# Kernel tuning notes

Measured on AMD Instinct MI355X. Metric: run time of the kernel, lower is better.

The kernel has to match this reference:

```python
import jax, jax.numpy as jnp
import numpy as np

B, C, H, W = 8, 512, 64, 64
DEPTH, HEADS = 4, 8


def setup_inputs() -> dict:
    key = jax.random.key(0)
    ks = jax.random.split(key, 7)
    s = 0.02
    return {
        "x": jax.random.normal(ks[0], (B, C, H, W), jnp.float32),
        # axial positional embeddings, emb dim at index 1: (1,C,H,1) and (1,C,1,W)
        "pos_h": jax.random.normal(ks[1], (C, H), jnp.float32) * s,
        "pos_w": jax.random.normal(ks[2], (C, W), jnp.float32) * s,
        # per layer, per axis (0=height, 1=width): q, kv, out projections
        "wq": jax.random.normal(ks[3], (DEPTH, 2, C, C), jnp.float32) * s,
        "wkv": jax.random.normal(ks[4], (DEPTH, 2, C, 2 * C), jnp.float32) * s,
        "wo": jax.random.normal(ks[5], (DEPTH, 2, C, C), jnp.float32) * s,
        "wo_b": jax.random.normal(ks[6], (DEPTH, 2, C), jnp.float32) * s,
    }


def _attn_last_axis(x, wq, wkv, wo, wo_b, heads):
    """Self-attention along the second-to-last axis. x: (..., L, C)."""
    lead = x.shape[:-2]
    L, Cd = x.shape[-2], x.shape[-1]
    e = Cd // heads
    q = x @ wq                       # (..., L, C)
    k, v = jnp.split(x @ wkv, 2, axis=-1)
    sh = lead + (L, heads, e)
    q, k, v = q.reshape(sh), k.reshape(sh), v.reshape(sh)
    dots = jnp.einsum('...ihe,...jhe->...hij', q, k) * (e ** -0.5)
    attn = jax.nn.softmax(dots, axis=-1)
    out = jnp.einsum('...hij,...jhe->...ihe', attn, v).reshape(lead + (L, heads * e))
    return out @ wo + wo_b


def reference(x, pos_h, pos_w, wq, wkv, wo, wo_b):
    # positional embedding: x + (1,C,H,1) + (1,C,1,W)
    x = x + pos_h[None, :, :, None] + pos_w[None, :, None, :]
    y = jnp.transpose(x, (0, 2, 3, 1))  # (B,H,W,C) channels-last working layout
    for l in range(DEPTH):
        # height-axis attention: (B,W,H,C), attend along H
        yh = jnp.transpose(y, (0, 2, 1, 3))
        oh = _attn_last_axis(yh, wq[l, 0], wkv[l, 0], wo[l, 0], wo_b[l, 0], HEADS)
        oh = jnp.transpose(oh, (0, 2, 1, 3))
        # width-axis attention: attend along W
        ow = _attn_last_axis(y, wq[l, 1], wkv[l, 1], wo[l, 1], wo_b[l, 1], HEADS)
        y = oh + ow  # sum_axial_out=True, no residual
    return jnp.transpose(y, (0, 3, 1, 2))  # back to (B,C,H,W)
```

## Files before the change

kernel.cpp:

```cpp
#include <hip/hip_runtime.h>
#include <stdint.h>


typedef __attribute__((ext_vector_type(8))) short bf16x8;
typedef __attribute__((ext_vector_type(4))) float f32x4;
typedef unsigned short u16;
typedef unsigned int u32;

#define MFMA16(a, b, c) __builtin_amdgcn_mfma_f32_16x16x32_bf16((a), (b), (c), 0, 0, 0)

__device__ __forceinline__ float b2f(u16 h) {
    u32 u = ((u32)h) << 16;
    float f;
    __builtin_memcpy(&f, &u, 4);
    return f;
}
__device__ __forceinline__ u16 f2b(float f) {
    u32 u;
    __builtin_memcpy(&u, &f, 4);
    u32 r = (u + 0x7fffu + ((u >> 16) & 1u)) >> 16;
    return (u16)r;
}

#define GLD_LDS16(g, l)                                                        \
    __builtin_amdgcn_global_load_lds(                                          \
        (const __attribute__((address_space(1))) void*)(g),                    \
        (__attribute__((address_space(3))) void*)(l), 16, 0, 0)

__global__ __launch_bounds__(256) void embed_kernel(
    const float* __restrict__ x, const float* __restrict__ ph,
    const float* __restrict__ pw, u16* __restrict__ y)
{
    __shared__ float tile[64][65];
    const int c0 = blockIdx.x * 64, h = blockIdx.y, b = blockIdx.z;
    const int t = threadIdx.x;
#pragma unroll
    for (int i = 0; i < 4; ++i) {
        int cl = (t >> 4) + i * 16;
        int w4 = (t & 15) * 4;
        const float* src = x + (((size_t)(b * 512 + c0 + cl)) * 64 + h) * 64 + w4;
        float4 v = *(const float4*)src;
        float p = ph[(c0 + cl) * 64 + h];
        tile[cl][w4 + 0] = v.x + p + pw[(c0 + cl) * 64 + w4 + 0];
        tile[cl][w4 + 1] = v.y + p + pw[(c0 + cl) * 64 + w4 + 1];
        tile[cl][w4 + 2] = v.z + p + pw[(c0 + cl) * 64 + w4 + 2];
        tile[cl][w4 + 3] = v.w + p + pw[(c0 + cl) * 64 + w4 + 3];
    }
    __syncthreads();
    const int wl = t >> 2, cb = (t & 3) * 16;
    bf16x8 o0, o1;
#pragma unroll
    for (int j = 0; j < 8; ++j) o0[j] = (short)f2b(tile[cb + j][wl]);
#pragma unroll
    for (int j = 0; j < 8; ++j) o1[j] = (short)f2b(tile[cb + 8 + j][wl]);
    u16* dst = y + (((size_t)(b * 64 + h) * 64 + wl) * 512 + c0 + cb);
    *(bf16x8*)dst = o0;
    *(bf16x8*)(dst + 8) = o1;
}

__global__ __launch_bounds__(256) void wtrans_kernel(
    const float* __restrict__ wq, const float* __restrict__ wkv,
    const float* __restrict__ wo, u16* __restrict__ wT)
{
    const int mid = blockIdx.z;
    const int l = mid / 6, rest = mid % 6, axis = rest / 3, which = rest % 3;
    const size_t la = (size_t)(l * 2 + axis);
    const float* src;
    int N;
    size_t doff;
    if (which == 0)      { src = wq  + la * 512 * 512;  N = 512;  doff = la * (2048 * 512); }
    else if (which == 1) { src = wkv + la * 512 * 1024; N = 1024; doff = la * (2048 * 512) + 512 * 512; }
    else                 { src = wo  + la * 512 * 512;  N = 512;  doff = la * (2048 * 512) + 512 * 512 + 1024 * 512; }
    const int n0 = blockIdx.y * 64;
    if (n0 >= N) return;
    const int k0 = blockIdx.x * 64;
    __shared__ float tile[64][65];
    const int t = threadIdx.x;
#pragma unroll
    for (int i = 0; i < 4; ++i) {
        int kl = (t >> 4) + i * 16;
        int n4 = (t & 15) * 4;
        float4 v = *(const float4*)(src + (size_t)(k0 + kl) * N + n0 + n4);
        tile[kl][n4 + 0] = v.x; tile[kl][n4 + 1] = v.y;
        tile[kl][n4 + 2] = v.z; tile[kl][n4 + 3] = v.w;
    }
    __syncthreads();
    const int nl = t >> 2, kb = (t & 3) * 16;
    bf16x8 o0, o1;
#pragma unroll
    for (int j = 0; j < 8; ++j) o0[j] = (short)f2b(tile[kb + j][nl]);
#pragma unroll
    for (int j = 0; j < 8; ++j) o1[j] = (short)f2b(tile[kb + 8 + j][nl]);
    u16* dst = wT + doff + (size_t)(n0 + nl) * 512 + k0 + kb;
    *(bf16x8*)dst = o0;
    *(bf16x8*)(dst + 8) = o1;
}

template <int MODE, int PERM>
__global__ __launch_bounds__(256) void gemm_bt(
    const u16* __restrict__ A, int lda,
    const u16* __restrict__ Bt,
    const float* __restrict__ bias,
    u16* C, int ldc)
{
    __shared__ u16 As[128 * 64];
    __shared__ u16 Bs[128 * 64];
    const int tid = threadIdx.x;
    const int lane = tid & 63;
    const int wv = tid >> 6;
    const int wr = (wv >> 1) * 64, wc = (wv & 1) * 64;
    const int nbx = gridDim.x;
    int lin = blockIdx.x + nbx * blockIdx.y;
    int cpx = (nbx * gridDim.y) >> 3;
    int id = (lin & 7) * cpx + (lin >> 3);
    const int n0 = (id % nbx) * 128;
    const int m0 = (id / nbx) * 128;
    const int rl = lane >> 3;
    const int cp = lane & 7;
    const int l16 = lane & 15;
    const int g = lane >> 4;
    const int kgrp = g << 3;
    f32x4 acc[4][4] = {};

    for (int ks = 0; ks < 512; ks += 64) {
#pragma unroll
        for (int i = 0; i < 4; ++i) {
            int row = wv * 8 + i * 32 + rl;
            int clog = cp ^ (row & 7);
            const u16* src = A + (size_t)(m0 + row) * lda + ks + clog * 8;
            GLD_LDS16(src, As + (wv * 8 + i * 32) * 64);
        }
#pragma unroll
        for (int i = 0; i < 4; ++i) {
            int row = wv * 8 + i * 32 + rl;
            int clog = cp ^ (row & 7);
            const u16* src = Bt + (size_t)(n0 + row) * 512 + ks + clog * 8;
            GLD_LDS16(src, Bs + (wv * 8 + i * 32) * 64);
        }
        __syncthreads();
#pragma unroll
        for (int kk = 0; kk < 2; ++kk) {
            bf16x8 af[4], bfr[4];
            const int kb = (kk * 32 + kgrp) * 2;
#pragma unroll
            for (int mf = 0; mf < 4; ++mf) {
                int row = wr + mf * 16 + l16;
                af[mf] = *(const bf16x8*)((const char*)As + row * 128 + (kb ^ ((row & 7) << 4)));
            }
#pragma unroll
            for (int nf = 0; nf < 4; ++nf) {
                int row = wc + nf * 16 + l16;
                bfr[nf] = *(const bf16x8*)((const char*)Bs + row * 128 + (kb ^ ((row & 7) << 4)));
            }
#pragma unroll
            for (int nf = 0; nf < 4; ++nf)
#pragma unroll
                for (int mf = 0; mf < 4; ++mf)
                    acc[nf][mf] = MFMA16(bfr[nf], af[mf], acc[nf][mf]);
        }
        __syncthreads();
    }

    float bv[4][4];
    if (MODE >= 1) {
#pragma unroll
        for (int nf = 0; nf < 4; ++nf) {
            float4 b4 = *(const float4*)(bias + n0 + wc + nf * 16 + g * 4);
            bv[nf][0] = b4.x; bv[nf][1] = b4.y; bv[nf][2] = b4.z; bv[nf][3] = b4.w;
        }
    }
#pragma unroll
    for (int mf = 0; mf < 4; ++mf) {
        const int m = m0 + wr + mf * 16 + l16;
        const int mp = PERM ? ((m & ~4095) | ((m & 63) << 6) | ((m >> 6) & 63)) : m;
        u16* crow = C + (size_t)mp * ldc;
#pragma unroll
        for (int nf = 0; nf < 4; ++nf) {
            const int n = n0 + wc + nf * 16 + g * 4;
            u16* cptr = crow + n;
            float v0 = acc[nf][mf][0], v1 = acc[nf][mf][1];
            float v2 = acc[nf][mf][2], v3 = acc[nf][mf][3];
            if (MODE >= 1) { v0 += bv[nf][0]; v1 += bv[nf][1]; v2 += bv[nf][2]; v3 += bv[nf][3]; }
            if (MODE == 2) {
                ushort4 o = *(const ushort4*)cptr;
                v0 += b2f(o.x); v1 += b2f(o.y); v2 += b2f(o.z); v3 += b2f(o.w);
            }
            uint2 pk;
            pk.x = (u32)f2b(v0) | ((u32)f2b(v1) << 16);
            pk.y = (u32)f2b(v2) | ((u32)f2b(v3) << 16);
            *(uint2*)cptr = pk;
        }
    }
}

__global__ __launch_bounds__(256) void attn_kernel(u16* QKV)
{
    __shared__ u16 sm[4][2][64 * 64];
    const int tid = threadIdx.x, lane = tid & 63, wv = tid >> 6;
    const int unit = blockIdx.x * 4 + wv;
    const int base = (unit >> 3) * 64;
    const int hoff = (unit & 7) * 64;
    const int l16 = lane & 15, g = lane >> 4;
    const int kgrp = g << 3;
    const int rl = lane >> 3, cp = lane & 7;
    u16* Kl = (u16*)sm[wv][0];
    u16* Vt = (u16*)sm[wv][1];

#pragma unroll
    for (int i = 0; i < 8; ++i) {
        int row = i * 8 + rl;
        int clog = cp ^ (row & 7);
        const u16* src = QKV + (size_t)(base + row) * 1536 + 512 + hoff + clog * 8;
        GLD_LDS16(src, Kl + i * 8 * 64);
    }
    bf16x8 q[4][2];
#pragma unroll
    for (int i_f = 0; i_f < 4; ++i_f)
#pragma unroll
        for (int k2 = 0; k2 < 2; ++k2)
            q[i_f][k2] = *(const bf16x8*)(QKV + (size_t)(base + i_f * 16 + l16) * 1536
                                          + hoff + k2 * 32 + kgrp);
    bf16x8 vvr[8];
#pragma unroll
    for (int i = 0; i < 8; ++i)
        vvr[i] = *(const bf16x8*)(QKV + (size_t)(base + i * 8 + rl) * 1536
                                  + 1024 + hoff + cp * 8);

    asm volatile("s_waitcnt vmcnt(0)" ::: "memory");
    __builtin_amdgcn_sched_barrier(0);

    f32x4 st[4][4] = {};
#pragma unroll
    for (int k2 = 0; k2 < 2; ++k2) {
        bf16x8 kf[4];
        const int kb = (k2 * 32 + kgrp) * 2;
#pragma unroll
        for (int j_f = 0; j_f < 4; ++j_f) {
            int row = j_f * 16 + l16;
            kf[j_f] = *(const bf16x8*)((const char*)Kl + row * 128 + (kb ^ ((row & 7) << 4)));
        }
#pragma unroll
        for (int i_f = 0; i_f < 4; ++i_f)
#pragma unroll
            for (int j_f = 0; j_f < 4; ++j_f)
                st[i_f][j_f] = MFMA16(kf[j_f], q[i_f][k2], st[i_f][j_f]);
    }

#pragma unroll
    for (int i = 0; i < 8; ++i) {
        int j2 = i * 16 + rl * 2;
#pragma unroll
        for (int t = 0; t < 8; ++t) {
            int e = cp * 8 + t;
            int addr = e * 128 + (j2 ^ (((t ^ cp) & 7) << 4));
            *(u16*)((char*)Vt + addr) = (u16)vvr[i][t];
        }
    }

#pragma unroll
    for (int i_f = 0; i_f < 4; ++i_f) {
        const int irow = i_f * 16 + l16;
        float ev[4][4];
        float mx = -1e30f;
#pragma unroll
        for (int j_f = 0; j_f < 4; ++j_f)
#pragma unroll
            for (int r = 0; r < 4; ++r) {
                float v = st[i_f][j_f][r] * 0.125f;
                ev[j_f][r] = v;
                mx = fmaxf(mx, v);
            }
        mx = fmaxf(mx, __shfl_xor(mx, 16, 64));
        mx = fmaxf(mx, __shfl_xor(mx, 32, 64));
        float sum = 0.f;
#pragma unroll
        for (int j_f = 0; j_f < 4; ++j_f)
#pragma unroll
            for (int r = 0; r < 4; ++r) {
                float e = __expf(ev[j_f][r] - mx);
                ev[j_f][r] = e;
                sum += e;
            }
        sum += __shfl_xor(sum, 16, 64);
        sum += __shfl_xor(sum, 32, 64);
        float inv = __builtin_amdgcn_rcpf(sum);
#pragma unroll
        for (int j_f = 0; j_f < 4; ++j_f) {
            uint2 pk;
            pk.x = (u32)f2b(ev[j_f][0] * inv) | ((u32)f2b(ev[j_f][1] * inv) << 16);
            pk.y = (u32)f2b(ev[j_f][2] * inv) | ((u32)f2b(ev[j_f][3] * inv) << 16);
            int addr = irow * 128 + ((j_f * 32 + g * 8) ^ ((irow & 7) << 4));
            *(uint2*)((char*)Kl + addr) = pk;
        }
    }

    f32x4 of[4][4] = {};
#pragma unroll
    for (int k2 = 0; k2 < 2; ++k2) {
        bf16x8 vf[4], pf[4];
        const int kb = (k2 * 32 + kgrp) * 2;
#pragma unroll
        for (int e_f = 0; e_f < 4; ++e_f) {
            int row = e_f * 16 + l16;
            int sw = ((row & 7) ^ ((row >> 3) & 7)) << 4;
            vf[e_f] = *(const bf16x8*)((const char*)Vt + row * 128 + (kb ^ sw));
        }
#pragma unroll
        for (int i_f = 0; i_f < 4; ++i_f) {
            int row = i_f * 16 + l16;
            pf[i_f] = *(const bf16x8*)((const char*)Kl + row * 128 + (kb ^ ((row & 7) << 4)));
        }
#pragma unroll
        for (int e_f = 0; e_f < 4; ++e_f)
#pragma unroll
            for (int i_f = 0; i_f < 4; ++i_f)
                of[e_f][i_f] = MFMA16(vf[e_f], pf[i_f], of[e_f][i_f]);
    }

#pragma unroll
    for (int i_f = 0; i_f < 4; ++i_f) {
        const int i = i_f * 16 + l16;
        u16* orow = QKV + (size_t)(base + i) * 1536 + hoff + g * 4;
#pragma unroll
        for (int e_f = 0; e_f < 4; ++e_f) {
            uint2 pk;
            pk.x = (u32)f2b(of[e_f][i_f][0]) | ((u32)f2b(of[e_f][i_f][1]) << 16);
            pk.y = (u32)f2b(of[e_f][i_f][2]) | ((u32)f2b(of[e_f][i_f][3]) << 16);
            *(uint2*)(orow + e_f * 16) = pk;
        }
    }
}

__global__ __launch_bounds__(256) void untrans_kernel(
    const u16* __restrict__ y, float* __restrict__ out)
{
    __shared__ float tile[64][65];
    const int c0 = blockIdx.x * 64, h = blockIdx.y, b = blockIdx.z;
    const int t = threadIdx.x;
    {
        const int wl = t >> 2, cb = (t & 3) * 16;
        const u16* src = y + (((size_t)(b * 64 + h) * 64 + wl) * 512 + c0 + cb);
        bf16x8 v0 = *(const bf16x8*)src;
        bf16x8 v1 = *(const bf16x8*)(src + 8);
#pragma unroll
        for (int j = 0; j < 8; ++j) tile[wl][cb + j] = b2f((u16)v0[j]);
#pragma unroll
        for (int j = 0; j < 8; ++j) tile[wl][cb + 8 + j] = b2f((u16)v1[j]);
    }
    __syncthreads();
    const int cl = t >> 2, w16 = (t & 3) * 16;
    float* dst = out + (((size_t)(b * 512 + c0 + cl)) * 64 + h) * 64 + w16;
#pragma unroll
    for (int j = 0; j < 4; ++j) {
        float4 v;
        v.x = tile[w16 + j * 4 + 0][cl];
        v.y = tile[w16 + j * 4 + 1][cl];
        v.z = tile[w16 + j * 4 + 2][cl];
        v.w = tile[w16 + j * 4 + 3][cl];
        *(float4*)(dst + j * 4) = v;
    }
}

extern "C" void kernel_launch(void* const* d_in, const int* in_sizes, int n_in,
                              void* d_out, int out_size, void* d_ws, size_t ws_size,
                              hipStream_t stream)
{
    (void)in_sizes; (void)n_in; (void)out_size; (void)ws_size;
    const float* x   = (const float*)d_in[0];
    const float* ph  = (const float*)d_in[1];
    const float* pw  = (const float*)d_in[2];
    const float* wq  = (const float*)d_in[3];
    const float* wkv = (const float*)d_in[4];
    const float* wo  = (const float*)d_in[5];
    const float* wob = (const float*)d_in[6];

    char* ws = (char*)d_ws;
    u16* yA  = (u16*)(ws);
    u16* yB  = (u16*)(ws + 33554432);
    u16* QKV = (u16*)(ws + 67108864);
    u16* wT  = (u16*)(ws + 167772160);
    float* out = (float*)d_out;

    embed_kernel<<<dim3(8, 64, 8), 256, 0, stream>>>(x, ph, pw, yA);
    wtrans_kernel<<<dim3(8, 16, 24), 256, 0, stream>>>(wq, wkv, wo, wT);

    u16* yin = yA;
    u16* yout = yB;
    for (int l = 0; l < 4; ++l) {
        for (int axis = 0; axis < 2; ++axis) {
            const u16* wTla = wT + (size_t)(l * 2 + axis) * 2048 * 512;
            const float* bias = wob + (size_t)(l * 2 + axis) * 512;
            const u16* woT = wTla + 512 * 512 + 1024 * 512;
            if (axis == 0)
                gemm_bt<0, 1><<<dim3(12, 256), 256, 0, stream>>>(yin, 512, wTla, nullptr, QKV, 1536);
            else
                gemm_bt<0, 0><<<dim3(12, 256), 256, 0, stream>>>(yin, 512, wTla, nullptr, QKV, 1536);
            attn_kernel<<<dim3(1024), 256, 0, stream>>>(QKV);
            if (axis == 0)
                gemm_bt<1, 1><<<dim3(4, 256), 256, 0, stream>>>(QKV, 1536, woT, bias, yout, 512);
            else
                gemm_bt<2, 0><<<dim3(4, 256), 256, 0, stream>>>(QKV, 1536, woT, bias, yout, 512);
        }
        u16* tmp = yin; yin = yout; yout = tmp;
    }
    untrans_kernel<<<dim3(8, 64, 8), 256, 0, stream>>>(yin, out);
}
```

Measured before the change: 1.181 ms.

## Replace GEMM with 256x256-tile double-buffered pipelined kernel

Swaps the 128x128 single-buffered GEMM for a 256x256 tile kernel with 8 waves, each computing 128x64 of output. LDS is double-buffered so global-to-LDS loads for the next K step run while MFMAs consume the current one, with explicit vmcnt waits and raw barriers. Fragment loads are split into phases and MFMA bursts are wrapped in setprio. The larger tile raises arithmetic intensity, but it uses 128KB of LDS per block, which limits occupancy. The grid also shrinks, which could hurt load balance on the smaller output projection.

```diff
diff --git a/kernel.cpp b/kernel.cpp
--- a/kernel.cpp
+++ b/kernel.cpp
@@ -97,86 +97,144 @@
 }
 
 template <int MODE, int PERM>
-__global__ __launch_bounds__(256) void gemm_bt(
+__global__ __launch_bounds__(512, 2) void gemm256(
     const u16* __restrict__ A, int lda,
     const u16* __restrict__ Bt,
     const float* __restrict__ bias,
     u16* C, int ldc)
 {
-    __shared__ u16 As[128 * 64];
-    __shared__ u16 Bs[128 * 64];
-    const int tid = threadIdx.x;
-    const int lane = tid & 63;
-    const int wv = tid >> 6;
-    const int wr = (wv >> 1) * 64, wc = (wv & 1) * 64;
-    const int nbx = gridDim.x;
-    int lin = blockIdx.x + nbx * blockIdx.y;
-    int cpx = (nbx * gridDim.y) >> 3;
+    __shared__ u16 As[2][256 * 64];
+    __shared__ u16 Bs[2][256 * 64];
+    const int tid = threadIdx.x, lane = tid & 63, wid = tid >> 6;
+    const int wm = wid >> 2, wn = wid & 3;
+    int lin = blockIdx.x + gridDim.x * blockIdx.y;
+    int cpx = (gridDim.x * gridDim.y) >> 3;
     int id = (lin & 7) * cpx + (lin >> 3);
-    const int n0 = (id % nbx) * 128;
-    const int m0 = (id / nbx) * 128;
-    const int rl = lane >> 3;
-    const int cp = lane & 7;
-    const int l16 = lane & 15;
-    const int g = lane >> 4;
+    const int n0 = (id % gridDim.x) * 256;
+    const int m0 = (id / gridDim.x) * 256;
+    const int rl = lane >> 3, cp = lane & 7, l16 = lane & 15, g = lane >> 4;
     const int kgrp = g << 3;
-    f32x4 acc[4][4] = {};
-
-    for (int ks = 0; ks < 512; ks += 64) {
-#pragma unroll
-        for (int i = 0; i < 4; ++i) {
-            int row = wv * 8 + i * 32 + rl;
-            int clog = cp ^ (row & 7);
-            const u16* src = A + (size_t)(m0 + row) * lda + ks + clog * 8;
-            GLD_LDS16(src, As + (wv * 8 + i * 32) * 64);
-        }
-#pragma unroll
-        for (int i = 0; i < 4; ++i) {
-            int row = wv * 8 + i * 32 + rl;
-            int clog = cp ^ (row & 7);
-            const u16* src = Bt + (size_t)(n0 + row) * 512 + ks + clog * 8;
-            GLD_LDS16(src, Bs + (wv * 8 + i * 32) * 64);
-        }
-        __syncthreads();
-#pragma unroll
-        for (int kk = 0; kk < 2; ++kk) {
-            bf16x8 af[4], bfr[4];
-            const int kb = (kk * 32 + kgrp) * 2;
-#pragma unroll
-            for (int mf = 0; mf < 4; ++mf) {
-                int row = wr + mf * 16 + l16;
-                af[mf] = *(const bf16x8*)((const char*)As + row * 128 + (kb ^ ((row & 7) << 4)));
-            }
-#pragma unroll
-            for (int nf = 0; nf < 4; ++nf) {
-                int row = wc + nf * 16 + l16;
-                bfr[nf] = *(const bf16x8*)((const char*)Bs + row * 128 + (kb ^ ((row & 7) << 4)));
-            }
-#pragma unroll
-            for (int nf = 0; nf < 4; ++nf)
+
+    f32x4 acc[4][8] = {};
+
+#define STAGE(b, ks)                                                           \
+    {                                                                          \
+        _Pragma("unroll")                                                      \
+        for (int j = 0; j < 4; ++j) {                                          \
+            int grp = wid + 8 * j;                                             \
+            int row = grp * 8 + rl;                                            \
+            const u16* s = A + (size_t)(m0 + row) * lda + (ks) + (cp ^ (row & 7)) * 8; \
+            GLD_LDS16(s, As[b] + grp * 512);                                   \
+        }                                                                      \
+        _Pragma("unroll")                                                      \
+        for (int j = 0; j < 4; ++j) {                                          \
+            int grp = wid + 8 * j;                                             \
+            int row = grp * 8 + rl;                                            \
+            const u16* s = Bt + (size_t)(n0 + row) * 512 + (ks) + (cp ^ (row & 7)) * 8; \
+            GLD_LDS16(s, Bs[b] + grp * 512);                                   \
+        }                                                                      \
+    }
+
+#define FRAG(base, row, kk)                                                    \
+    (*(const bf16x8*)((const char*)(base) + (row) * 128 +                      \
+                      (((kk) * 64 + g * 16) ^ (((row) & 7) << 4))))
+
+    STAGE(0, 0);
+
+    for (int t = 0; t < 8; ++t) {
+        const int cb = t & 1;
+        if (t < 7) STAGE(cb ^ 1, (t + 1) * 64);
+        __builtin_amdgcn_sched_barrier(0);
+        if (t < 7) { asm volatile("s_waitcnt vmcnt(8)" ::: "memory"); }
+        else       { asm volatile("s_waitcnt vmcnt(0)" ::: "memory"); }
+        __builtin_amdgcn_s_barrier();
+        __builtin_amdgcn_sched_barrier(0);
+
+        const u16* cA = As[cb];
+        const u16* cB = Bs[cb];
+        bf16x8 bl[2][2], bh[2][2], af[4][2];
+
+#pragma unroll
+        for (int nf = 0; nf < 2; ++nf)
+#pragma unroll
+            for (int kk = 0; kk < 2; ++kk)
+                bl[nf][kk] = FRAG(cB, wn * 64 + nf * 16 + l16, kk);
+#pragma unroll
+        for (int mf = 0; mf < 4; ++mf)
+#pragma unroll
+            for (int kk = 0; kk < 2; ++kk)
+                af[mf][kk] = FRAG(cA, wm * 128 + mf * 16 + l16, kk);
+        __builtin_amdgcn_s_setprio(1);
+#pragma unroll
+        for (int kk = 0; kk < 2; ++kk)
+#pragma unroll
+            for (int nf = 0; nf < 2; ++nf)
 #pragma unroll
                 for (int mf = 0; mf < 4; ++mf)
-                    acc[nf][mf] = MFMA16(bfr[nf], af[mf], acc[nf][mf]);
-        }
-        __syncthreads();
+                    acc[nf][mf] = MFMA16(bl[nf][kk], af[mf][kk], acc[nf][mf]);
+        __builtin_amdgcn_s_setprio(0);
+
+#pragma unroll
+        for (int nf = 0; nf < 2; ++nf)
+#pragma unroll
+            for (int kk = 0; kk < 2; ++kk)
+                bh[nf][kk] = FRAG(cB, wn * 64 + 32 + nf * 16 + l16, kk);
+        __builtin_amdgcn_s_setprio(1);
+#pragma unroll
+        for (int kk = 0; kk < 2; ++kk)
+#pragma unroll
+            for (int nf = 0; nf < 2; ++nf)
+#pragma unroll
+                for (int mf = 0; mf < 4; ++mf)
+                    acc[2 + nf][mf] = MFMA16(bh[nf][kk], af[mf][kk], acc[2 + nf][mf]);
+        __builtin_amdgcn_s_setprio(0);
+
+#pragma unroll
+        for (int mf = 0; mf < 4; ++mf)
+#pragma unroll
+            for (int kk = 0; kk < 2; ++kk)
+                af[mf][kk] = FRAG(cA, wm * 128 + 64 + mf * 16 + l16, kk);
+        __builtin_amdgcn_s_setprio(1);
+#pragma unroll
+        for (int kk = 0; kk < 2; ++kk)
+#pragma unroll
+            for (int nf = 0; nf < 2; ++nf)
+#pragma unroll
+                for (int mf = 0; mf < 4; ++mf)
+                    acc[2 + nf][4 + mf] = MFMA16(bh[nf][kk], af[mf][kk], acc[2 + nf][4 + mf]);
+        __builtin_amdgcn_s_setprio(0);
+
+        __builtin_amdgcn_s_setprio(1);
+#pragma unroll
+        for (int kk = 0; kk < 2; ++kk)
+#pragma unroll
+            for (int nf = 0; nf < 2; ++nf)
+#pragma unroll
+                for (int mf = 0; mf < 4; ++mf)
+                    acc[nf][4 + mf] = MFMA16(bl[nf][kk], af[mf][kk], acc[nf][4 + mf]);
+        __builtin_amdgcn_s_setprio(0);
+
+        __builtin_amdgcn_sched_barrier(0);
+        __builtin_amdgcn_s_barrier();
+        __builtin_amdgcn_sched_barrier(0);
     }
 
     float bv[4][4];
     if (MODE >= 1) {
 #pragma unroll
         for (int nf = 0; nf < 4; ++nf) {
-            float4 b4 = *(const float4*)(bias + n0 + wc + nf * 16 + g * 4);
+            float4 b4 = *(const float4*)(bias + n0 + wn * 64 + nf * 16 + g * 4);
             bv[nf][0] = b4.x; bv[nf][1] = b4.y; bv[nf][2] = b4.z; bv[nf][3] = b4.w;
         }
     }
 #pragma unroll
-    for (int mf = 0; mf < 4; ++mf) {
-        const int m = m0 + wr + mf * 16 + l16;
+    for (int mf = 0; mf < 8; ++mf) {
+        const int m = m0 + wm * 128 + mf * 16 + l16;
         const int mp = PERM ? ((m & ~4095) | ((m & 63) << 6) | ((m >> 6) & 63)) : m;
         u16* crow = C + (size_t)mp * ldc;
 #pragma unroll
         for (int nf = 0; nf < 4; ++nf) {
-            const int n = n0 + wc + nf * 16 + g * 4;
+            const int n = n0 + wn * 64 + nf * 16 + g * 4;
             u16* cptr = crow + n;
             float v0 = acc[nf][mf][0], v1 = acc[nf][mf][1];
             float v2 = acc[nf][mf][2], v3 = acc[nf][mf][3];
@@ -191,6 +249,8 @@
             *(uint2*)cptr = pk;
         }
     }
+#undef STAGE
+#undef FRAG
 }
 
 __global__ __launch_bounds__(256) void attn_kernel(u16* QKV)
@@ -392,14 +452,14 @@
             const float* bias = wob + (size_t)(l * 2 + axis) * 512;
             const u16* woT = wTla + 512 * 512 + 1024 * 512;
             if (axis == 0)
-                gemm_bt<0, 1><<<dim3(12, 256), 256, 0, stream>>>(yin, 512, wTla, nullptr, QKV, 1536);
+                gemm256<0, 1><<<dim3(6, 128), 512, 0, stream>>>(yin, 512, wTla, nullptr, QKV, 1536);
             else
-                gemm_bt<0, 0><<<dim3(12, 256), 256, 0, stream>>>(yin, 512, wTla, nullptr, QKV, 1536);
+                gemm256<0, 0><<<dim3(6, 128), 512, 0, stream>>>(yin, 512, wTla, nullptr, QKV, 1536);
             attn_kernel<<<dim3(1024), 256, 0, stream>>>(QKV);
             if (axis == 0)
-                gemm_bt<1, 1><<<dim3(4, 256), 256, 0, stream>>>(QKV, 1536, woT, bias, yout, 512);
+                gemm256<1, 1><<<dim3(2, 128), 512, 0, stream>>>(QKV, 1536, woT, bias, yout, 512);
             else
-                gemm_bt<2, 0><<<dim3(4, 256), 256, 0, stream>>>(QKV, 1536, woT, bias, yout, 512);
+                gemm256<2, 0><<<dim3(2, 128), 512, 0, stream>>>(QKV, 1536, woT, bias, yout, 512);
         }
         u16* tmp = yin; yin = yout; yout = tmp;
     }
```

New measurement: 1.076 ms. 8.9% less time.

## Fuse QKV projection, axial attention, and output projection into one kernel per axis

Applied to the files above, without the earlier changes.

Replaces the three-kernel sequence (QKV GEMM, attention, output GEMM) with a single kernel per axis. Each 512-thread block loads one 64-row sequence into LDS, and each wave computes one head's Q/K/V projections, softmax attention and a slice of the output projection. This removes the large QKV intermediate buffer round-trip through global memory and two kernel launches per axis. In exchange, weight fragments are read directly from global memory without LDS staging, and with only 512 blocks weights are re-read per block, so memory or latency bound behaviour may change.

```diff
diff --git a/kernel.cpp b/kernel.cpp
--- a/kernel.cpp
+++ b/kernel.cpp
@@ -8,6 +8,7 @@
 typedef unsigned int u32;
 
 #define MFMA16(a, b, c) __builtin_amdgcn_mfma_f32_16x16x32_bf16((a), (b), (c), 0, 0, 0)
+#define SBAR() __builtin_amdgcn_sched_barrier(0)
 
 __device__ __forceinline__ float b2f(u16 h) {
     u32 u = ((u32)h) << 16;
@@ -20,6 +21,12 @@
     __builtin_memcpy(&u, &f, 4);
     u32 r = (u + 0x7fffu + ((u >> 16) & 1u)) >> 16;
     return (u16)r;
+}
+__device__ __forceinline__ uint2 pack4(const f32x4& v) {
+    uint2 pk;
+    pk.x = (u32)f2b(v[0]) | ((u32)f2b(v[1]) << 16);
+    pk.y = (u32)f2b(v[2]) | ((u32)f2b(v[3]) << 16);
+    return pk;
 }
 
 #define GLD_LDS16(g, l)                                                        \
@@ -96,166 +103,100 @@
     *(bf16x8*)(dst + 8) = o1;
 }
 
-template <int MODE, int PERM>
-__global__ __launch_bounds__(256) void gemm_bt(
-    const u16* __restrict__ A, int lda,
-    const u16* __restrict__ Bt,
+template <int AXIS>
+__global__ __launch_bounds__(512, 2) void fused_layer(
+    const u16* __restrict__ y,
+    const u16* __restrict__ wTla,
     const float* __restrict__ bias,
-    u16* C, int ldc)
+    u16* __restrict__ yout)
 {
-    __shared__ u16 As[128 * 64];
-    __shared__ u16 Bs[128 * 64];
-    const int tid = threadIdx.x;
-    const int lane = tid & 63;
-    const int wv = tid >> 6;
-    const int wr = (wv >> 1) * 64, wc = (wv & 1) * 64;
-    const int nbx = gridDim.x;
-    int lin = blockIdx.x + nbx * blockIdx.y;
-    int cpx = (nbx * gridDim.y) >> 3;
-    int id = (lin & 7) * cpx + (lin >> 3);
-    const int n0 = (id % nbx) * 128;
-    const int m0 = (id / nbx) * 128;
-    const int rl = lane >> 3;
-    const int cp = lane & 7;
-    const int l16 = lane & 15;
-    const int g = lane >> 4;
-    const int kgrp = g << 3;
-    f32x4 acc[4][4] = {};
-
-    for (int ks = 0; ks < 512; ks += 64) {
-#pragma unroll
-        for (int i = 0; i < 4; ++i) {
-            int row = wv * 8 + i * 32 + rl;
-            int clog = cp ^ (row & 7);
-            const u16* src = A + (size_t)(m0 + row) * lda + ks + clog * 8;
-            GLD_LDS16(src, As + (wv * 8 + i * 32) * 64);
-        }
-#pragma unroll
-        for (int i = 0; i < 4; ++i) {
-            int row = wv * 8 + i * 32 + rl;
-            int clog = cp ^ (row & 7);
-            const u16* src = Bt + (size_t)(n0 + row) * 512 + ks + clog * 8;
-            GLD_LDS16(src, Bs + (wv * 8 + i * 32) * 64);
-        }
-        __syncthreads();
-#pragma unroll
-        for (int kk = 0; kk < 2; ++kk) {
-            bf16x8 af[4], bfr[4];
-            const int kb = (kk * 32 + kgrp) * 2;
-#pragma unroll
-            for (int mf = 0; mf < 4; ++mf) {
-                int row = wr + mf * 16 + l16;
-                af[mf] = *(const bf16x8*)((const char*)As + row * 128 + (kb ^ ((row & 7) << 4)));
+    __shared__ u16 LDS[65536];
+    const int tid = threadIdx.x, lane = tid & 63, wid = tid >> 6;
+    const int l16 = lane & 15, g = lane >> 4;
+    const int bid = blockIdx.x;
+    const size_t rowbase = ((size_t)(bid >> 6) << 12) +
+                           (AXIS == 0 ? (size_t)(bid & 63) : ((size_t)(bid & 63) << 6));
+    const int rowstr = (AXIS == 0) ? 64 : 1;
+
+    u16* Ys = LDS;
+    u16* scr = LDS + 32768 + wid * 4096;
+
+#pragma unroll
+    for (int i = 0; i < 8; ++i) {
+        int row = wid * 8 + i;
+        const u16* src = y + (rowbase + (size_t)row * rowstr) * 512 + ((lane ^ (row & 7)) << 3);
+        GLD_LDS16(src, Ys + row * 512);
+    }
+    __syncthreads();
+
+    const int hoff = wid * 64;
+    const u16* wq_ = wTla + (size_t)hoff * 512;
+    const u16* wk_ = wTla + (size_t)(512 + hoff) * 512;
+    const u16* wv_ = wTla + (size_t)(512 + 512 + hoff) * 512;
+    const u16* wo_ = wTla + (size_t)(512 + 1024) * 512;
+
+#define YF(r, t) (*(const bf16x8*)((const char*)Ys + (r) * 1024 + \
+                    ((((t) * 4 + g) ^ ((r) & 7)) << 4)))
+#define SF(r, k2) (*(const bf16x8*)((const char*)scr + (r) * 128 + \
+                    (((k2) * 64 + g * 16) ^ (((r) & 7) << 4))))
+
+    f32x4 ak[4][4] = {}, aq[4][4] = {};
+#pragma unroll
+    for (int t = 0; t < 16; ++t) {
+        bf16x8 yf[4], wkf[4], wqf[4];
+#pragma unroll
+        for (int f = 0; f < 4; ++f) {
+            int row = f * 16 + l16;
+            yf[f]  = YF(row, t);
+            wkf[f] = *(const bf16x8*)(wk_ + (size_t)row * 512 + t * 32 + g * 8);
+            wqf[f] = *(const bf16x8*)(wq_ + (size_t)row * 512 + t * 32 + g * 8);
+        }
+#pragma unroll
+        for (int ef = 0; ef < 4; ++ef)
+#pragma unroll
+            for (int jf = 0; jf < 4; ++jf) {
+                ak[ef][jf] = MFMA16(wkf[ef], yf[jf], ak[ef][jf]);
+                aq[ef][jf] = MFMA16(wqf[ef], yf[jf], aq[ef][jf]);
             }
-#pragma unroll
-            for (int nf = 0; nf < 4; ++nf) {
-                int row = wc + nf * 16 + l16;
-                bfr[nf] = *(const bf16x8*)((const char*)Bs + row * 128 + (kb ^ ((row & 7) << 4)));
-            }
-#pragma unroll
-            for (int nf = 0; nf < 4; ++nf)
-#pragma unroll
-                for (int mf = 0; mf < 4; ++mf)
-                    acc[nf][mf] = MFMA16(bfr[nf], af[mf], acc[nf][mf]);
-        }
-        __syncthreads();
-    }
-
-    float bv[4][4];
-    if (MODE >= 1) {
-#pragma unroll
-        for (int nf = 0; nf < 4; ++nf) {
-            float4 b4 = *(const float4*)(bias + n0 + wc + nf * 16 + g * 4);
-            bv[nf][0] = b4.x; bv[nf][1] = b4.y; bv[nf][2] = b4.z; bv[nf][3] = b4.w;
-        }
-    }
-#pragma unroll
-    for (int mf = 0; mf < 4; ++mf) {
-        const int m = m0 + wr + mf * 16 + l16;
-        const int mp = PERM ? ((m & ~4095) | ((m & 63) << 6) | ((m >> 6) & 63)) : m;
-        u16* crow = C + (size_t)mp * ldc;
-#pragma unroll
-        for (int nf = 0; nf < 4; ++nf) {
-            const int n = n0 + wc + nf * 16 + g * 4;
-            u16* cptr = crow + n;
-            float v0 = acc[nf][mf][0], v1 = acc[nf][mf][1];
-            float v2 = acc[nf][mf][2], v3 = acc[nf][mf][3];
-            if (MODE >= 1) { v0 += bv[nf][0]; v1 += bv[nf][1]; v2 += bv[nf][2]; v3 += bv[nf][3]; }
-            if (MODE == 2) {
-                ushort4 o = *(const ushort4*)cptr;
-                v0 += b2f(o.x); v1 += b2f(o.y); v2 += b2f(o.z); v3 += b2f(o.w);
-            }
-            uint2 pk;
-            pk.x = (u32)f2b(v0) | ((u32)f2b(v1) << 16);
-            pk.y = (u32)f2b(v2) | ((u32)f2b(v3) << 16);
-            *(uint2*)cptr = pk;
-        }
-    }
-}
-
-__global__ __launch_bounds__(256) void attn_kernel(u16* QKV)
-{
-    __shared__ u16 sm[4][2][64 * 64];
-    const int tid = threadIdx.x, lane = tid & 63, wv = tid >> 6;
-    const int unit = blockIdx.x * 4 + wv;
-    const int base = (unit >> 3) * 64;
-    const int hoff = (unit & 7) * 64;
-    const int l16 = lane & 15, g = lane >> 4;
-    const int kgrp = g << 3;
-    const int rl = lane >> 3, cp = lane & 7;
-    u16* Kl = (u16*)sm[wv][0];
-    u16* Vt = (u16*)sm[wv][1];
-
-#pragma unroll
-    for (int i = 0; i < 8; ++i) {
-        int row = i * 8 + rl;
-        int clog = cp ^ (row & 7);
-        const u16* src = QKV + (size_t)(base + row) * 1536 + 512 + hoff + clog * 8;
-        GLD_LDS16(src, Kl + i * 8 * 64);
-    }
-    bf16x8 q[4][2];
-#pragma unroll
-    for (int i_f = 0; i_f < 4; ++i_f)
-#pragma unroll
-        for (int k2 = 0; k2 < 2; ++k2)
-            q[i_f][k2] = *(const bf16x8*)(QKV + (size_t)(base + i_f * 16 + l16) * 1536
-                                          + hoff + k2 * 32 + kgrp);
-    bf16x8 vvr[8];
-#pragma unroll
-    for (int i = 0; i < 8; ++i)
-        vvr[i] = *(const bf16x8*)(QKV + (size_t)(base + i * 8 + rl) * 1536
-                                  + 1024 + hoff + cp * 8);
-
-    asm volatile("s_waitcnt vmcnt(0)" ::: "memory");
-    __builtin_amdgcn_sched_barrier(0);
+    }
+
+#pragma unroll
+    for (int ef = 0; ef < 4; ++ef)
+#pragma unroll
+        for (int jf = 0; jf < 4; ++jf) {
+            int j = jf * 16 + l16, bo = (ef * 16 + g * 4) * 2;
+            *(uint2*)((char*)scr + j * 128 + (bo ^ ((j & 7) << 4))) = pack4(ak[ef][jf]);
+        }
+    SBAR();
+    bf16x8 kf[4][2];
+#pragma unroll
+    for (int jf = 0; jf < 4; ++jf)
+#pragma unroll
+        for (int k2 = 0; k2 < 2; ++k2) kf[jf][k2] = SF(jf * 16 + l16, k2);
+    SBAR();
+#pragma unroll
+    for (int ef = 0; ef < 4; ++ef)
+#pragma unroll
+        for (int jf = 0; jf < 4; ++jf) {
+            int j = jf * 16 + l16, bo = (ef * 16 + g * 4) * 2;
+            *(uint2*)((char*)scr + j * 128 + (bo ^ ((j & 7) << 4))) = pack4(aq[ef][jf]);
+        }
+    SBAR();
+    bf16x8 qf[4][2];
+#pragma unroll
+    for (int if_ = 0; if_ < 4; ++if_)
+#pragma unroll
+        for (int k2 = 0; k2 < 2; ++k2) qf[if_][k2] = SF(if_ * 16 + l16, k2);
+    SBAR();
 
     f32x4 st[4][4] = {};
 #pragma unroll
-    for (int k2 = 0; k2 < 2; ++k2) {
-        bf16x8 kf[4];
-        const int kb = (k2 * 32 + kgrp) * 2;
-#pragma unroll
-        for (int j_f = 0; j_f < 4; ++j_f) {
-            int row = j_f * 16 + l16;
-            kf[j_f] = *(const bf16x8*)((const char*)Kl + row * 128 + (kb ^ ((row & 7) << 4)));
-        }
+    for (int k2 = 0; k2 < 2; ++k2)
 #pragma unroll
         for (int i_f = 0; i_f < 4; ++i_f)
 #pragma unroll
             for (int j_f = 0; j_f < 4; ++j_f)
-                st[i_f][j_f] = MFMA16(kf[j_f], q[i_f][k2], st[i_f][j_f]);
-    }
-
-#pragma unroll
-    for (int i = 0; i < 8; ++i) {
-        int j2 = i * 16 + rl * 2;
-#pragma unroll
-        for (int t = 0; t < 8; ++t) {
-            int e = cp * 8 + t;
-            int addr = e * 128 + (j2 ^ (((t ^ cp) & 7) << 4));
-            *(u16*)((char*)Vt + addr) = (u16)vvr[i][t];
-        }
-    }
+                st[i_f][j_f] = MFMA16(kf[j_f][k2], qf[i_f][k2], st[i_f][j_f]);
 
 #pragma unroll
     for (int i_f = 0; i_f < 4; ++i_f) {
@@ -290,45 +231,112 @@
             pk.x = (u32)f2b(ev[j_f][0] * inv) | ((u32)f2b(ev[j_f][1] * inv) << 16);
             pk.y = (u32)f2b(ev[j_f][2] * inv) | ((u32)f2b(ev[j_f][3] * inv) << 16);
             int addr = irow * 128 + ((j_f * 32 + g * 8) ^ ((irow & 7) << 4));
-            *(uint2*)((char*)Kl + addr) = pk;
-        }
-    }
+            *(uint2*)((char*)scr + addr) = pk;
+        }
+    }
+    SBAR();
+    bf16x8 pf[4][2];
+#pragma unroll
+    for (int if_ = 0; if_ < 4; ++if_)
+#pragma unroll
+        for (int k2 = 0; k2 < 2; ++k2) pf[if_][k2] = SF(if_ * 16 + l16, k2);
+    SBAR();
+
+    f32x4 av[4][4] = {};
+#pragma unroll
+    for (int t = 0; t < 16; ++t) {
+        bf16x8 yf[4], wvf[4];
+#pragma unroll
+        for (int f = 0; f < 4; ++f) {
+            int row = f * 16 + l16;
+            yf[f]  = YF(row, t);
+            wvf[f] = *(const bf16x8*)(wv_ + (size_t)row * 512 + t * 32 + g * 8);
+        }
+#pragma unroll
+        for (int jf = 0; jf < 4; ++jf)
+#pragma unroll
+            for (int ef = 0; ef < 4; ++ef)
+                av[jf][ef] = MFMA16(yf[jf], wvf[ef], av[jf][ef]);
+    }
+#pragma unroll
+    for (int jf = 0; jf < 4; ++jf)
+#pragma unroll
+        for (int ef = 0; ef < 4; ++ef) {
+            int e = ef * 16 + l16, bo = (jf * 16 + g * 4) * 2;
+            *(uint2*)((char*)scr + e * 128 + (bo ^ ((e & 7) << 4))) = pack4(av[jf][ef]);
+        }
+    SBAR();
+    bf16x8 vtf[4][2];
+#pragma unroll
+    for (int ef = 0; ef < 4; ++ef)
+#pragma unroll
+        for (int k2 = 0; k2 < 2; ++k2) vtf[ef][k2] = SF(ef * 16 + l16, k2);
+    SBAR();
 
     f32x4 of[4][4] = {};
 #pragma unroll
-    for (int k2 = 0; k2 < 2; ++k2) {
-        bf16x8 vf[4], pf[4];
-        const int kb = (k2 * 32 + kgrp) * 2;
-#pragma unroll
-        for (int e_f = 0; e_f < 4; ++e_f) {
-            int row = e_f * 16 + l16;
-            int sw = ((row & 7) ^ ((row >> 3) & 7)) << 4;
-            vf[e_f] = *(const bf16x8*)((const char*)Vt + row * 128 + (kb ^ sw));
-        }
+    for (int k2 = 0; k2 < 2; ++k2)
+#pragma unroll
+        for (int ef = 0; ef < 4; ++ef)
+#pragma unroll
+            for (int i_f = 0; i_f < 4; ++i_f)
+                of[ef][i_f] = MFMA16(vtf[ef][k2], pf[i_f][k2], of[ef][i_f]);
+
+    __syncthreads();
+#pragma unroll
+    for (int ef = 0; ef < 4; ++ef)
 #pragma unroll
         for (int i_f = 0; i_f < 4; ++i_f) {
-            int row = i_f * 16 + l16;
-            pf[i_f] = *(const bf16x8*)((const char*)Kl + row * 128 + (kb ^ ((row & 7) << 4)));
-        }
-#pragma unroll
-        for (int e_f = 0; e_f < 4; ++e_f)
-#pragma unroll
-            for (int i_f = 0; i_f < 4; ++i_f)
-                of[e_f][i_f] = MFMA16(vf[e_f], pf[i_f], of[e_f][i_f]);
-    }
-
-#pragma unroll
-    for (int i_f = 0; i_f < 4; ++i_f) {
-        const int i = i_f * 16 + l16;
-        u16* orow = QKV + (size_t)(base + i) * 1536 + hoff + g * 4;
-#pragma unroll
-        for (int e_f = 0; e_f < 4; ++e_f) {
+            int i = i_f * 16 + l16;
+            int bo = (hoff + ef * 16 + g * 4) * 2;
+            *(uint2*)((char*)Ys + i * 1024 + (bo ^ ((i & 7) << 4))) = pack4(of[ef][i_f]);
+        }
+    __syncthreads();
+
+    const int n0 = hoff;
+    f32x4 ao[4][4] = {};
+#pragma unroll
+    for (int t = 0; t < 16; ++t) {
+        bf16x8 off[4], wof[4];
+#pragma unroll
+        for (int f = 0; f < 4; ++f) {
+            int row = f * 16 + l16;
+            off[f] = YF(row, t);
+            wof[f] = *(const bf16x8*)(wo_ + (size_t)(n0 + row) * 512 + t * 32 + g * 8);
+        }
+#pragma unroll
+        for (int nf = 0; nf < 4; ++nf)
+#pragma unroll
+            for (int if_ = 0; if_ < 4; ++if_)
+                ao[nf][if_] = MFMA16(wof[nf], off[if_], ao[nf][if_]);
+    }
+
+    float4 b4[4];
+#pragma unroll
+    for (int nf = 0; nf < 4; ++nf) b4[nf] = *(const float4*)(bias + n0 + nf * 16 + g * 4);
+#pragma unroll
+    for (int if_ = 0; if_ < 4; ++if_) {
+        const int i = if_ * 16 + l16;
+        u16* dst = yout + (rowbase + (size_t)i * rowstr) * 512;
+#pragma unroll
+        for (int nf = 0; nf < 4; ++nf) {
+            const int n = n0 + nf * 16 + g * 4;
+            float v0 = ao[nf][if_][0] + b4[nf].x;
+            float v1 = ao[nf][if_][1] + b4[nf].y;
+            float v2 = ao[nf][if_][2] + b4[nf].z;
+            float v3 = ao[nf][if_][3] + b4[nf].w;
+            if (AXIS == 1) {
+                ushort4 o = *(const ushort4*)(dst + n);
+                v0 += b2f(o.x); v1 += b2f(o.y); v2 += b2f(o.z); v3 += b2f(o.w);
+            }
             uint2 pk;
-            pk.x = (u32)f2b(of[e_f][i_f][0]) | ((u32)f2b(of[e_f][i_f][1]) << 16);
-            pk.y = (u32)f2b(of[e_f][i_f][2]) | ((u32)f2b(of[e_f][i_f][3]) << 16);
-            *(uint2*)(orow + e_f * 16) = pk;
-        }
-    }
+            pk.x = (u32)f2b(v0) | ((u32)f2b(v1) << 16);
+            pk.y = (u32)f2b(v2) | ((u32)f2b(v3) << 16);
+            *(uint2*)(dst + n) = pk;
+        }
+    }
+#undef YF
+#undef SF
 }
 
 __global__ __launch_bounds__(256) void untrans_kernel(
@@ -375,10 +383,9 @@
     const float* wob = (const float*)d_in[6];
 
     char* ws = (char*)d_ws;
-    u16* yA  = (u16*)(ws);
-    u16* yB  = (u16*)(ws + 33554432);
-    u16* QKV = (u16*)(ws + 67108864);
-    u16* wT  = (u16*)(ws + 167772160);
+    u16* yA = (u16*)(ws);
+    u16* yB = (u16*)(ws + 33554432);
+    u16* wT = (u16*)(ws + 67108864);
     float* out = (float*)d_out;
 
     embed_kernel<<<dim3(8, 64, 8), 256, 0, stream>>>(x, ph, pw, yA);
@@ -390,16 +397,10 @@
         for (int axis = 0; axis < 2; ++axis) {
             const u16* wTla = wT + (size_t)(l * 2 + axis) * 2048 * 512;
             const float* bias = wob + (size_t)(l * 2 + axis) * 512;
-            const u16* woT = wTla + 512 * 512 + 1024 * 512;
             if (axis == 0)
-                gemm_bt<0, 1><<<dim3(12, 256), 256, 0, stream>>>(yin, 512, wTla, nullptr, QKV, 1536);
+                fused_layer<0><<<dim3(512), 512, 0, stream>>>(yin, wTla, bias, yout);
             else
-                gemm_bt<0, 0><<<dim3(12, 256), 256, 0, stream>>>(yin, 512, wTla, nullptr, QKV, 1536);
-            attn_kernel<<<dim3(1024), 256, 0, stream>>>(QKV);
-            if (axis == 0)
-                gemm_bt<1, 1><<<dim3(4, 256), 256, 0, stream>>>(QKV, 1536, woT, bias, yout, 512);
-            else
-                gemm_bt<2, 0><<<dim3(4, 256), 256, 0, stream>>>(QKV, 1536, woT, bias, yout, 512);
+                fused_layer<1><<<dim3(512), 512, 0, stream>>>(yin, wTla, bias, yout);
         }
         u16* tmp = yin; yin = yout; yout = tmp;
     }
```

Measured after the change: 1.222 ms. +3.5%, slower.

## Replace tiled GEMM with persistent row-strip GEMM using 4-stage LDS ring prefetch

Applied to the files above, without the earlier changes.

Replaces the one-tile-per-block bf16 GEMM with a kernel that launches one 512-thread block per 128-row strip and walks every N tile in sequence. Operands stream through a 4-deep LDS ring filled by global_load_lds two stages ahead, with explicit vmcnt waits, a single barrier per stage, and raised wave priority around the MFMA block. Each tile's epilogue is written out and the accumulators reset inside the loop. The aim is to overlap global loads with MFMA work and remove per-block launch and prologue cost, at the price of about 128KB of LDS per block, lower occupancy and no reuse of A across N tiles.

```diff
diff --git a/kernel.cpp b/kernel.cpp
--- a/kernel.cpp
+++ b/kernel.cpp
@@ -8,6 +8,7 @@
 typedef unsigned int u32;
 
 #define MFMA16(a, b, c) __builtin_amdgcn_mfma_f32_16x16x32_bf16((a), (b), (c), 0, 0, 0)
+#define SBAR() __builtin_amdgcn_sched_barrier(0)
 
 __device__ __forceinline__ float b2f(u16 h) {
     u32 u = ((u32)h) << 16;
@@ -20,6 +21,12 @@
     __builtin_memcpy(&u, &f, 4);
     u32 r = (u + 0x7fffu + ((u >> 16) & 1u)) >> 16;
     return (u16)r;
+}
+__device__ __forceinline__ uint2 pack4(const f32x4& v) {
+    uint2 pk;
+    pk.x = (u32)f2b(v[0]) | ((u32)f2b(v[1]) << 16);
+    pk.y = (u32)f2b(v[2]) | ((u32)f2b(v[3]) << 16);
+    return pk;
 }
 
 #define GLD_LDS16(g, l)                                                        \
@@ -96,101 +103,122 @@
     *(bf16x8*)(dst + 8) = o1;
 }
 
-template <int MODE, int PERM>
-__global__ __launch_bounds__(256) void gemm_bt(
+template <int MODE, int PERM, int NSUB>
+__global__ __launch_bounds__(512, 2) void gemm_ring(
     const u16* __restrict__ A, int lda,
     const u16* __restrict__ Bt,
     const float* __restrict__ bias,
     u16* C, int ldc)
 {
-    __shared__ u16 As[128 * 64];
-    __shared__ u16 Bs[128 * 64];
-    const int tid = threadIdx.x;
-    const int lane = tid & 63;
-    const int wv = tid >> 6;
-    const int wr = (wv >> 1) * 64, wc = (wv & 1) * 64;
-    const int nbx = gridDim.x;
-    int lin = blockIdx.x + nbx * blockIdx.y;
-    int cpx = (nbx * gridDim.y) >> 3;
-    int id = (lin & 7) * cpx + (lin >> 3);
-    const int n0 = (id % nbx) * 128;
-    const int m0 = (id / nbx) * 128;
-    const int rl = lane >> 3;
-    const int cp = lane & 7;
-    const int l16 = lane & 15;
-    const int g = lane >> 4;
-    const int kgrp = g << 3;
-    f32x4 acc[4][4] = {};
-
-    for (int ks = 0; ks < 512; ks += 64) {
-#pragma unroll
-        for (int i = 0; i < 4; ++i) {
-            int row = wv * 8 + i * 32 + rl;
-            int clog = cp ^ (row & 7);
-            const u16* src = A + (size_t)(m0 + row) * lda + ks + clog * 8;
-            GLD_LDS16(src, As + (wv * 8 + i * 32) * 64);
-        }
-#pragma unroll
-        for (int i = 0; i < 4; ++i) {
-            int row = wv * 8 + i * 32 + rl;
-            int clog = cp ^ (row & 7);
-            const u16* src = Bt + (size_t)(n0 + row) * 512 + ks + clog * 8;
-            GLD_LDS16(src, Bs + (wv * 8 + i * 32) * 64);
-        }
-        __syncthreads();
-#pragma unroll
-        for (int kk = 0; kk < 2; ++kk) {
-            bf16x8 af[4], bfr[4];
-            const int kb = (kk * 32 + kgrp) * 2;
-#pragma unroll
-            for (int mf = 0; mf < 4; ++mf) {
-                int row = wr + mf * 16 + l16;
-                af[mf] = *(const bf16x8*)((const char*)As + row * 128 + (kb ^ ((row & 7) << 4)));
+    __shared__ u16 As[4][128 * 64];
+    __shared__ u16 Bs[4][128 * 64];
+    const int tid = threadIdx.x, lane = tid & 63, wid = tid >> 6;
+    const int wm = wid >> 1, wn = wid & 1;
+    const int rl = lane >> 3, cp = lane & 7, l16 = lane & 15, g = lane >> 4;
+    const int bp = (blockIdx.x & 7) * 32 + (blockIdx.x >> 3);
+    const int m0 = bp * 128;
+    const int S = NSUB * 8;
+
+    f32x4 acc[4][2] = {};
+
+#define STAGE(r, s2)                                                           \
+    {                                                                          \
+        const int n0s = ((s2) >> 3) * 128;                                     \
+        const int ks = ((s2) & 7) * 64;                                        \
+        _Pragma("unroll")                                                      \
+        for (int j = 0; j < 2; ++j) {                                          \
+            int row = j * 64 + wid * 8 + rl;                                   \
+            const u16* s_ = A + (size_t)(m0 + row) * lda + ks + (cp ^ (row & 7)) * 8; \
+            GLD_LDS16(s_, As[r] + (j * 64 + wid * 8) * 64);                    \
+        }                                                                      \
+        _Pragma("unroll")                                                      \
+        for (int j = 0; j < 2; ++j) {                                          \
+            int row = j * 64 + wid * 8 + rl;                                   \
+            const u16* s_ = Bt + (size_t)(n0s + row) * 512 + ks + (cp ^ (row & 7)) * 8; \
+            GLD_LDS16(s_, Bs[r] + (j * 64 + wid * 8) * 64);                    \
+        }                                                                      \
+    }
+
+#define FRAG(base, row, kk)                                                    \
+    (*(const bf16x8*)((const char*)(base) + (row) * 128 +                      \
+                      (((kk) * 64 + g * 16) ^ (((row) & 7) << 4))))
+
+    STAGE(0, 0);
+    STAGE(1, 1);
+
+    for (int s = 0; s < S; ++s) {
+        if (s + 2 < S) {
+            STAGE((s + 2) & 3, s + 2);
+            __builtin_amdgcn_sched_barrier(0);
+            asm volatile("s_waitcnt vmcnt(8)" ::: "memory");
+        } else if (s + 1 < S) {
+            asm volatile("s_waitcnt vmcnt(4)" ::: "memory");
+        } else {
+            asm volatile("s_waitcnt vmcnt(0)" ::: "memory");
+        }
+        __builtin_amdgcn_s_barrier();
+        __builtin_amdgcn_sched_barrier(0);
+
+        const u16* cA = As[s & 3];
+        const u16* cB = Bs[s & 3];
+        bf16x8 af[2][2], bf[4][2];
+#pragma unroll
+        for (int mf = 0; mf < 2; ++mf)
+#pragma unroll
+            for (int kk = 0; kk < 2; ++kk)
+                af[mf][kk] = FRAG(cA, wm * 32 + mf * 16 + l16, kk);
+#pragma unroll
+        for (int nf = 0; nf < 4; ++nf)
+#pragma unroll
+            for (int kk = 0; kk < 2; ++kk)
+                bf[nf][kk] = FRAG(cB, wn * 64 + nf * 16 + l16, kk);
+        __builtin_amdgcn_s_setprio(1);
+#pragma unroll
+        for (int kk = 0; kk < 2; ++kk)
+#pragma unroll
+            for (int nf = 0; nf < 4; ++nf)
+#pragma unroll
+                for (int mf = 0; mf < 2; ++mf)
+                    acc[nf][mf] = MFMA16(bf[nf][kk], af[mf][kk], acc[nf][mf]);
+        __builtin_amdgcn_s_setprio(0);
+
+        if ((s & 7) == 7) {
+            const int n0 = (s >> 3) * 128;
+            float bv[4][4];
+            if (MODE >= 1) {
+#pragma unroll
+                for (int nf = 0; nf < 4; ++nf) {
+                    float4 b4 = *(const float4*)(bias + n0 + wn * 64 + nf * 16 + g * 4);
+                    bv[nf][0] = b4.x; bv[nf][1] = b4.y; bv[nf][2] = b4.z; bv[nf][3] = b4.w;
+                }
             }
 #pragma unroll
-            for (int nf = 0; nf < 4; ++nf) {
-                int row = wc + nf * 16 + l16;
-                bfr[nf] = *(const bf16x8*)((const char*)Bs + row * 128 + (kb ^ ((row & 7) << 4)));
+            for (int mf = 0; mf < 2; ++mf) {
+                const int m = m0 + wm * 32 + mf * 16 + l16;
+                const int mp = PERM ? ((m & ~4095) | ((m & 63) << 6) | ((m >> 6) & 63)) : m;
+                u16* crow = C + (size_t)mp * ldc;
+#pragma unroll
+                for (int nf = 0; nf < 4; ++nf) {
+                    const int n = n0 + wn * 64 + nf * 16 + g * 4;
+                    u16* cptr = crow + n;
+                    float v0 = acc[nf][mf][0], v1 = acc[nf][mf][1];
+                    float v2 = acc[nf][mf][2], v3 = acc[nf][mf][3];
+                    if (MODE >= 1) { v0 += bv[nf][0]; v1 += bv[nf][1]; v2 += bv[nf][2]; v3 += bv[nf][3]; }
+                    if (MODE == 2) {
+                        ushort4 o = *(const ushort4*)cptr;
+                        v0 += b2f(o.x); v1 += b2f(o.y); v2 += b2f(o.z); v3 += b2f(o.w);
+                    }
+                    uint2 pk;
+                    pk.x = (u32)f2b(v0) | ((u32)f2b(v1) << 16);
+                    pk.y = (u32)f2b(v2) | ((u32)f2b(v3) << 16);
+                    *(uint2*)cptr = pk;
+                    acc[nf][mf] = f32x4{0.f, 0.f, 0.f, 0.f};
+                }
             }
-#pragma unroll
-            for (int nf = 0; nf < 4; ++nf)
-#pragma unroll
-                for (int mf = 0; mf < 4; ++mf)
-                    acc[nf][mf] = MFMA16(bfr[nf], af[mf], acc[nf][mf]);
-        }
-        __syncthreads();
-    }
-
-    float bv[4][4];
-    if (MODE >= 1) {
-#pragma unroll
-        for (int nf = 0; nf < 4; ++nf) {
-            float4 b4 = *(const float4*)(bias + n0 + wc + nf * 16 + g * 4);
-            bv[nf][0] = b4.x; bv[nf][1] = b4.y; bv[nf][2] = b4.z; bv[nf][3] = b4.w;
-        }
-    }
-#pragma unroll
-    for (int mf = 0; mf < 4; ++mf) {
-        const int m = m0 + wr + mf * 16 + l16;
-        const int mp = PERM ? ((m & ~4095) | ((m & 63) << 6) | ((m >> 6) & 63)) : m;
-        u16* crow = C + (size_t)mp * ldc;
-#pragma unroll
-        for (int nf = 0; nf < 4; ++nf) {
-            const int n = n0 + wc + nf * 16 + g * 4;
-            u16* cptr = crow + n;
-            float v0 = acc[nf][mf][0], v1 = acc[nf][mf][1];
-            float v2 = acc[nf][mf][2], v3 = acc[nf][mf][3];
-            if (MODE >= 1) { v0 += bv[nf][0]; v1 += bv[nf][1]; v2 += bv[nf][2]; v3 += bv[nf][3]; }
-            if (MODE == 2) {
-                ushort4 o = *(const ushort4*)cptr;
-                v0 += b2f(o.x); v1 += b2f(o.y); v2 += b2f(o.z); v3 += b2f(o.w);
-            }
-            uint2 pk;
-            pk.x = (u32)f2b(v0) | ((u32)f2b(v1) << 16);
-            pk.y = (u32)f2b(v2) | ((u32)f2b(v3) << 16);
-            *(uint2*)cptr = pk;
-        }
-    }
+        }
+    }
+#undef STAGE
+#undef FRAG
 }
 
 __global__ __launch_bounds__(256) void attn_kernel(u16* QKV)
@@ -257,6 +285,8 @@
         }
     }
 
+    bf16x8 pf[4][2];
+    (void)pf;
 #pragma unroll
     for (int i_f = 0; i_f < 4; ++i_f) {
         const int irow = i_f * 16 + l16;
@@ -297,7 +327,7 @@
     f32x4 of[4][4] = {};
 #pragma unroll
     for (int k2 = 0; k2 < 2; ++k2) {
-        bf16x8 vf[4], pf[4];
+        bf16x8 vf[4], pfr[4];
         const int kb = (k2 * 32 + kgrp) * 2;
 #pragma unroll
         for (int e_f = 0; e_f < 4; ++e_f) {
@@ -308,13 +338,13 @@
 #pragma unroll
         for (int i_f = 0; i_f < 4; ++i_f) {
             int row = i_f * 16 + l16;
-            pf[i_f] = *(const bf16x8*)((const char*)Kl + row * 128 + (kb ^ ((row & 7) << 4)));
+            pfr[i_f] = *(const bf16x8*)((const char*)Kl + row * 128 + (kb ^ ((row & 7) << 4)));
         }
 #pragma unroll
         for (int e_f = 0; e_f < 4; ++e_f)
 #pragma unroll
             for (int i_f = 0; i_f < 4; ++i_f)
-                of[e_f][i_f] = MFMA16(vf[e_f], pf[i_f], of[e_f][i_f]);
+                of[e_f][i_f] = MFMA16(vf[e_f], pfr[i_f], of[e_f][i_f]);
     }
 
 #pragma unroll
@@ -392,14 +422,14 @@
             const float* bias = wob + (size_t)(l * 2 + axis) * 512;
             const u16* woT = wTla + 512 * 512 + 1024 * 512;
             if (axis == 0)
-                gemm_bt<0, 1><<<dim3(12, 256), 256, 0, stream>>>(yin, 512, wTla, nullptr, QKV, 1536);
+                gemm_ring<0, 1, 12><<<dim3(256), 512, 0, stream>>>(yin, 512, wTla, nullptr, QKV, 1536);
             else
-                gemm_bt<0, 0><<<dim3(12, 256), 256, 0, stream>>>(yin, 512, wTla, nullptr, QKV, 1536);
+                gemm_ring<0, 0, 12><<<dim3(256), 512, 0, stream>>>(yin, 512, wTla, nullptr, QKV, 1536);
             attn_kernel<<<dim3(1024), 256, 0, stream>>>(QKV);
             if (axis == 0)
-                gemm_bt<1, 1><<<dim3(4, 256), 256, 0, stream>>>(QKV, 1536, woT, bias, yout, 512);
+                gemm_ring<1, 1, 4><<<dim3(256), 512, 0, stream>>>(QKV, 1536, woT, bias, yout, 512);
             else
-                gemm_bt<2, 0><<<dim3(4, 256), 256, 0, stream>>>(QKV, 1536, woT, bias, yout, 512);
+                gemm_ring<2, 0, 4><<<dim3(256), 512, 0, stream>>>(QKV, 1536, woT, bias, yout, 512);
         }
         u16* tmp = yin; yin = yout; yout = tmp;
     }
```

Result: slower. 1.324 ms (+12.1%).
